# Kernel tuning notes

Measured on AMD Instinct MI355X. Metric: run time of the kernel, lower is better.

## Reference

```python
import jax, jax.numpy as jnp
import numpy as np

IN_DIM = 784   # 28*28
OUT_DIM = 16
NUM = 5        # grid intervals
K = 3          # spline order
HEADS = 10


def _make_grid():
    # pykan extended grid: linspace(-1,1,NUM+1) extended by K knots on each side
    h = 2.0 / NUM
    pts = np.arange(-K, NUM + K + 1, dtype=np.float32) * h - 1.0  # [NUM+2K+1]=12
    return jnp.asarray(np.broadcast_to(pts, (IN_DIM, pts.shape[0])))


def setup_inputs() -> dict:
    key = jax.random.key(0)
    ks = jax.random.split(key, 6)
    B = 16384
    x = jax.random.normal(ks[0], (B, 1, 28, 28), jnp.float32)
    grid = _make_grid()                                             # [784,12] (buffer)
    coef = jax.random.normal(ks[1], (HEADS, IN_DIM, OUT_DIM, NUM + K), jnp.float32) * 0.1
    scale_base = jax.random.normal(ks[2], (HEADS, IN_DIM, OUT_DIM), jnp.float32) * 0.1
    scale_sp = jnp.ones((HEADS, IN_DIM, OUT_DIM), jnp.float32)
    mask = jnp.ones((HEADS, IN_DIM, OUT_DIM), jnp.float32)
    w1 = jax.random.normal(ks[3], (HEADS, 8, OUT_DIM), jnp.float32) / np.sqrt(OUT_DIM)
    b1 = jnp.zeros((HEADS, 8), jnp.float32)
    w2 = jax.random.normal(ks[4], (HEADS, 1, 8), jnp.float32) / np.sqrt(8.0)
    b2 = jnp.zeros((HEADS, 1), jnp.float32)
    return dict(x=x, grid=grid, coef=coef, scale_base=scale_base, scale_sp=scale_sp,
                mask=mask, w1=w1, b1=b1, w2=w2, b2=b2)


def _b_spline(x, grid, k):
    # x: [B, D], grid: [D, G] -> bases [B, D, G-k-1] (Cox-de Boor recursion, pykan B_batch)
    xg = x[:, :, None]
    g = grid[None]
    B = ((xg >= g[:, :, :-1]) & (xg < g[:, :, 1:])).astype(x.dtype)
    for p in range(1, k + 1):
        left = (xg - g[:, :, :-(p + 1)]) / (g[:, :, p:-1] - g[:, :, :-(p + 1)])
        right = (g[:, :, p + 1:] - xg) / (g[:, :, p + 1:] - g[:, :, 1:-p])
        B = left * B[:, :, :-1] + right * B[:, :, 1:]
    return jnp.nan_to_num(B)


def reference(x, grid, coef, scale_base, scale_sp, mask, w1, b1, w2, b2):
    xf = x.reshape(x.shape[0], -1)                  # [B, 784]
    Bsp = _b_spline(xf, grid, K)                    # [B, 784, NUM+K]
    # KANLayer: y = sum_d mask*(scale_base*silu(x) + scale_sp*spline). Sum over d is
    # linear, so fold (scale_sp*mask) into coef to avoid the [B,H,784,16] intermediate.
    eff_coef = coef * (scale_sp * mask)[..., None]  # [H, 784, 16, NUM+K]
    y_sp = jnp.einsum('bdg,hdog->bho', Bsp, eff_coef)
    y_base = jnp.einsum('bd,hdo->bho', jax.nn.silu(xf), scale_base * mask)
    y = jnp.tanh(y_base + y_sp)                     # [B, H, 16] (nn.Tanh)
    h1 = jnp.tanh(jnp.einsum('bho,hpo->bhp', y, w1) + b1[None])   # Linear(16,8)+Tanh
    out = jnp.einsum('bhp,hqp->bhq', h1, w2) + b2[None]           # Linear(8,1)
    return out[..., 0]                              # concat of 10 heads -> [B, 10]
```

## Files before the change

### kernel.cpp

```cpp
#include <hip/hip_runtime.h>

#define IN_DIM 784
#define NF 9
#define NDB 25
#define NKC 225
#define KPAD (NKC*32)
#define BATCH 16384
#define NOUTC 160
#define NTILES 10
#define HEADS 10
#define KSPLIT 4
#define ROWB 576
#define CHUNKB 36864

typedef __attribute__((ext_vector_type(8))) short bf16x8;
typedef __attribute__((ext_vector_type(4))) float f32x4;
typedef __attribute__((ext_vector_type(4))) unsigned int u32x4;

__device__ __forceinline__ unsigned short f2bf(float f) {
    unsigned u = __builtin_bit_cast(unsigned, f);
    unsigned r = 0x7FFFu + ((u >> 16) & 1u);
    return (unsigned short)((u + r) >> 16);
}

__global__ void k_wprep(const float* __restrict__ coef, const float* __restrict__ scale_base,
                        const float* __restrict__ scale_sp, const float* __restrict__ mask,
                        unsigned short* __restrict__ Wp) {
    int tid = blockIdx.x * blockDim.x + threadIdx.x;
    if (tid >= KPAD * NOUTC) return;
    int frag = tid >> 9;
    int rem  = tid & 511;
    int l = rem >> 3, j = rem & 7;
    int kc = frag / NTILES, nt = frag - kc * NTILES;
    int db = kc / 9, c = kc - db * 9;
    int kk = ((l >> 4) << 3) + j;
    int d = db * 32 + kk;
    int n = nt * 16 + (l & 15);
    float v = 0.f;
    if (d < IN_DIM) {
        int h = n >> 4, o = n & 15;
        size_t base = ((size_t)h * IN_DIM + d) * 16 + o;
        float m = mask[base];
        v = (c == 0) ? scale_base[base] * m
                     : coef[base * 8 + (c - 1)] * scale_sp[base] * m;
    }
    Wp[tid] = f2bf(v);
}

template<int W>
__device__ __forceinline__ void do_units(const bf16x8* __restrict__ Bd,
                                         const char* __restrict__ lds,
                                         int q, int rr, f32x4* acc) {
    #pragma unroll
    for (int c = 0; c < 9; ++c) {
        bf16x8 aF[4];
        #pragma unroll
        for (int rg = 0; rg < 4; ++rg)
            aF[rg] = *(const bf16x8*)(lds + (rg * 16 + rr) * ROWB + c * 64 + q * 16);
        bf16x8 bcur;
        #pragma unroll
        for (int i = 0; i < 10; ++i) {
            const int tau = W * 10 + i;
            const int nt = tau >> 2, rg = tau & 3;
            if (i == 0 || rg == 0) bcur = Bd[c * (NTILES * 64) + nt * 64];
            acc[i] = __builtin_amdgcn_mfma_f32_16x16x32_bf16(aF[rg], bcur, acc[i], 0, 0, 0);
        }
    }
}

template<int W>
__device__ __forceinline__ void cwrite(float* __restrict__ pp, int row0g,
                                       int q, int rr, const f32x4* acc) {
    #pragma unroll
    for (int i = 0; i < 10; ++i) {
        const int tau = W * 10 + i;
        const int nt = tau >> 2, rg = tau & 3;
        #pragma unroll
        for (int ii = 0; ii < 4; ++ii)
            pp[(size_t)(row0g + rg * 16 + q * 4 + ii) * NOUTC + nt * 16 + rr] = acc[i][ii];
    }
}

__global__ void __launch_bounds__(256, 4) k_fused(const float* __restrict__ x,
                                                  const float* __restrict__ gridp,
                                                  const unsigned short* __restrict__ Wp,
                                                  float* __restrict__ part) {
    __shared__ char ldsb[CHUNKB];
    const int tid = threadIdx.x;
    const int l = tid & 63, wid = tid >> 6;
    const int q = l >> 4, rr = l & 15;
    const int row0g = blockIdx.x * 64;
    const int y = blockIdx.y;
    const int db0 = (y * NDB) >> 2, db1 = ((y + 1) * NDB) >> 2;

    const float g0 = gridp[0];
    const float ih = 1.f / (gridp[1] - g0);

    f32x4 acc[10];
    #pragma unroll
    for (int i = 0; i < 10; ++i) acc[i] = (f32x4){0.f, 0.f, 0.f, 0.f};

    const bf16x8* Bl = (const bf16x8*)Wp + l;
    const int sd = tid & 31;
    const int srow0 = tid >> 5;

    for (int db = db0; db < db1; ++db) {
        const u32x4 z = (u32x4){0u, 0u, 0u, 0u};
        #pragma unroll
        for (int i2 = 0; i2 < 9; ++i2) ((u32x4*)ldsb)[i2 * 256 + tid] = z;
        __syncthreads();

        const int d = db * 32 + sd;
        const bool valid = d < IN_DIM;
        #pragma unroll 4
        for (int it = 0; it < 8; ++it) {
            const int row = it * 8 + srow0;
            float xv = 0.f;
            if (valid) xv = x[(size_t)(row0g + row) * IN_DIM + d];
            const float u = (xv - g0) * ih;
            const float fm = floorf(u);
            const int m = (int)fm;
            const float t = u - fm;
            const float k6 = 0.16666667f;
            const float w0 = t * t * t * k6;
            const float w1 = fmaf(fmaf(fmaf(-3.f, t, 3.f), t, 3.f), t, 1.f) * k6;
            const float w2 = fmaf(fmaf(3.f, t, -6.f) * t, t, 4.f) * k6;
            const float omt = 1.f - t;
            const float w3 = omt * omt * omt * k6;
            const float den = 1.f + __expf(-xv);
            float inv; asm("v_rcp_f32 %0, %1" : "=v"(inv) : "v"(den));
            const float sil = xv * inv;
            if (valid) {
                char* rp = ldsb + row * ROWB;
                *(unsigned short*)(rp + sd * 2) = f2bf(sil);
                #pragma unroll
                for (int s = 0; s < 4; ++s) {
                    const int j = m - s;
                    const float w = (s == 0) ? w0 : (s == 1) ? w1 : (s == 2) ? w2 : w3;
                    if ((unsigned)j <= 7u)
                        *(unsigned short*)(rp + (j + 1) * 64 + sd * 2) = f2bf(w);
                }
            }
        }
        __syncthreads();

        const bf16x8* Bd = Bl + (size_t)db * (9 * NTILES * 64);
        switch (wid) {
            case 0:  do_units<0>(Bd, ldsb, q, rr, acc); break;
            case 1:  do_units<1>(Bd, ldsb, q, rr, acc); break;
            case 2:  do_units<2>(Bd, ldsb, q, rr, acc); break;
            default: do_units<3>(Bd, ldsb, q, rr, acc); break;
        }
        __syncthreads();
    }

    float* pp = part + (size_t)y * BATCH * NOUTC;
    switch (wid) {
        case 0:  cwrite<0>(pp, row0g, q, rr, acc); break;
        case 1:  cwrite<1>(pp, row0g, q, rr, acc); break;
        case 2:  cwrite<2>(pp, row0g, q, rr, acc); break;
        default: cwrite<3>(pp, row0g, q, rr, acc); break;
    }
}

__global__ void k_epi(const float* __restrict__ part, const float* __restrict__ w1,
                      const float* __restrict__ b1, const float* __restrict__ w2,
                      const float* __restrict__ b2, float* __restrict__ out) {
    int t = blockIdx.x * blockDim.x + threadIdx.x;
    if (t >= BATCH * HEADS) return;
    int b = t / HEADS;
    int h = t - b * HEADS;
    const f32x4* P = (const f32x4*)part;
    const int vbase = b * (NOUTC / 4) + h * 4;
    float y[16];
    #pragma unroll
    for (int c4 = 0; c4 < 4; ++c4) {
        f32x4 v = P[vbase + c4];
        #pragma unroll
        for (int s = 1; s < KSPLIT; ++s) {
            f32x4 v2 = P[(size_t)s * BATCH * (NOUTC / 4) + vbase + c4];
            v.x += v2.x; v.y += v2.y; v.z += v2.z; v.w += v2.w;
        }
        y[c4 * 4 + 0] = tanhf(v.x); y[c4 * 4 + 1] = tanhf(v.y);
        y[c4 * 4 + 2] = tanhf(v.z); y[c4 * 4 + 3] = tanhf(v.w);
    }
    float oacc = b2[h];
    #pragma unroll
    for (int p = 0; p < 8; ++p) {
        float a = b1[h * 8 + p];
        const float* wr = w1 + ((size_t)h * 8 + p) * 16;
        #pragma unroll
        for (int o = 0; o < 16; ++o) a = fmaf(y[o], wr[o], a);
        oacc = fmaf(tanhf(a), w2[h * 8 + p], oacc);
    }
    out[t] = oacc;
}

extern "C" void kernel_launch(void* const* d_in, const int* in_sizes, int n_in,
                              void* d_out, int out_size, void* d_ws, size_t ws_size,
                              hipStream_t stream) {
    const float* x          = (const float*)d_in[0];
    const float* gridp      = (const float*)d_in[1];
    const float* coef       = (const float*)d_in[2];
    const float* scale_base = (const float*)d_in[3];
    const float* scale_sp   = (const float*)d_in[4];
    const float* mask       = (const float*)d_in[5];
    const float* w1         = (const float*)d_in[6];
    const float* b1         = (const float*)d_in[7];
    const float* w2         = (const float*)d_in[8];
    const float* b2         = (const float*)d_in[9];
    float* out = (float*)d_out;

    char* ws = (char*)d_ws;
    float* part        = (float*)ws;
    unsigned short* Wp = (unsigned short*)(ws + 41943040);

    k_wprep<<<dim3((KPAD * NOUTC + 255) / 256), dim3(256), 0, stream>>>(coef, scale_base, scale_sp, mask, Wp);
    k_fused<<<dim3(BATCH / 64, KSPLIT), dim3(256), 0, stream>>>(x, gridp, Wp, part);
    k_epi  <<<dim3((BATCH * HEADS + 255) / 256), dim3(256), 0, stream>>>(part, w1, b1, w2, b2, out);
}
```

Measured before the change: 106.5 us.

## Switch to 32x32x16 MFMA with intra-block K-split across two waves

Replaces the 16x16x32 MFMA tiling over four waves with 32x32x16 MFMAs on two waves, each wave handling half of every 32-wide K chunk and all 160 outputs for 64 rows. The partial sums of the two waves are reduced through LDS before the global store. The weight prep is reordered to the new fragment layout and has the 1/6 spline constant folded in, which removes the per-element scaling. LDS rows are padded to reduce bank conflicts. Block size drops to 128 threads with larger accumulators per thread, which trades occupancy for fewer B-fragment loads and fewer MFMA issues.

```diff
diff --git a/kernel.cpp b/kernel.cpp
--- a/kernel.cpp
+++ b/kernel.cpp
@@ -1,20 +1,18 @@
 #include <hip/hip_runtime.h>
 
 #define IN_DIM 784
-#define NF 9
 #define NDB 25
-#define NKC 225
-#define KPAD (NKC*32)
+#define NUNITS (NDB*9)
 #define BATCH 16384
 #define NOUTC 160
-#define NTILES 10
 #define HEADS 10
 #define KSPLIT 4
-#define ROWB 576
-#define CHUNKB 36864
+#define ROWB 584
+#define CHUNKB (64*ROWB)
 
 typedef __attribute__((ext_vector_type(8))) short bf16x8;
 typedef __attribute__((ext_vector_type(4))) float f32x4;
+typedef __attribute__((ext_vector_type(16))) float f32x16;
 typedef __attribute__((ext_vector_type(4))) unsigned int u32x4;
 
 __device__ __forceinline__ unsigned short f2bf(float f) {
@@ -27,68 +25,36 @@
                         const float* __restrict__ scale_sp, const float* __restrict__ mask,
                         unsigned short* __restrict__ Wp) {
     int tid = blockIdx.x * blockDim.x + threadIdx.x;
-    if (tid >= KPAD * NOUTC) return;
+    if (tid >= NUNITS * 32 * NOUTC) return;
     int frag = tid >> 9;
     int rem  = tid & 511;
     int l = rem >> 3, j = rem & 7;
-    int kc = frag / NTILES, nt = frag - kc * NTILES;
+    int nt = frag % 5;
+    int t2 = frag / 5;
+    int kh = t2 & 1;
+    int kc = t2 >> 1;
     int db = kc / 9, c = kc - db * 9;
-    int kk = ((l >> 4) << 3) + j;
-    int d = db * 32 + kk;
-    int n = nt * 16 + (l & 15);
+    int d = db * 32 + kh * 16 + ((l >> 5) << 3) + j;
+    int n = nt * 32 + (l & 31);
     float v = 0.f;
     if (d < IN_DIM) {
         int h = n >> 4, o = n & 15;
         size_t base = ((size_t)h * IN_DIM + d) * 16 + o;
         float m = mask[base];
         v = (c == 0) ? scale_base[base] * m
-                     : coef[base * 8 + (c - 1)] * scale_sp[base] * m;
+                     : coef[base * 8 + (c - 1)] * scale_sp[base] * m * 0.16666667f;
     }
     Wp[tid] = f2bf(v);
 }
 
-template<int W>
-__device__ __forceinline__ void do_units(const bf16x8* __restrict__ Bd,
-                                         const char* __restrict__ lds,
-                                         int q, int rr, f32x4* acc) {
-    #pragma unroll
-    for (int c = 0; c < 9; ++c) {
-        bf16x8 aF[4];
-        #pragma unroll
-        for (int rg = 0; rg < 4; ++rg)
-            aF[rg] = *(const bf16x8*)(lds + (rg * 16 + rr) * ROWB + c * 64 + q * 16);
-        bf16x8 bcur;
-        #pragma unroll
-        for (int i = 0; i < 10; ++i) {
-            const int tau = W * 10 + i;
-            const int nt = tau >> 2, rg = tau & 3;
-            if (i == 0 || rg == 0) bcur = Bd[c * (NTILES * 64) + nt * 64];
-            acc[i] = __builtin_amdgcn_mfma_f32_16x16x32_bf16(aF[rg], bcur, acc[i], 0, 0, 0);
-        }
-    }
-}
-
-template<int W>
-__device__ __forceinline__ void cwrite(float* __restrict__ pp, int row0g,
-                                       int q, int rr, const f32x4* acc) {
-    #pragma unroll
-    for (int i = 0; i < 10; ++i) {
-        const int tau = W * 10 + i;
-        const int nt = tau >> 2, rg = tau & 3;
-        #pragma unroll
-        for (int ii = 0; ii < 4; ++ii)
-            pp[(size_t)(row0g + rg * 16 + q * 4 + ii) * NOUTC + nt * 16 + rr] = acc[i][ii];
-    }
-}
-
-__global__ void __launch_bounds__(256, 4) k_fused(const float* __restrict__ x,
+__global__ void __launch_bounds__(128, 2) k_fused(const float* __restrict__ x,
                                                   const float* __restrict__ gridp,
                                                   const unsigned short* __restrict__ Wp,
                                                   float* __restrict__ part) {
     __shared__ char ldsb[CHUNKB];
     const int tid = threadIdx.x;
-    const int l = tid & 63, wid = tid >> 6;
-    const int q = l >> 4, rr = l & 15;
+    const int l = tid & 63, kh = tid >> 6;
+    const int la = l & 31, lb = l >> 5;
     const int row0g = blockIdx.x * 64;
     const int y = blockIdx.y;
     const int db0 = (y * NDB) >> 2, db1 = ((y + 1) * NDB) >> 2;
@@ -96,37 +62,43 @@
     const float g0 = gridp[0];
     const float ih = 1.f / (gridp[1] - g0);
 
-    f32x4 acc[10];
+    f32x16 acc0[5], acc1[5];
     #pragma unroll
-    for (int i = 0; i < 10; ++i) acc[i] = (f32x4){0.f, 0.f, 0.f, 0.f};
-
-    const bf16x8* Bl = (const bf16x8*)Wp + l;
+    for (int i = 0; i < 5; ++i) {
+        #pragma unroll
+        for (int jj = 0; jj < 16; ++jj) { acc0[i][jj] = 0.f; acc1[i][jj] = 0.f; }
+    }
+
     const int sd = tid & 31;
     const int srow0 = tid >> 5;
+    const char* aAddr = ldsb + la * ROWB + kh * 32 + lb * 16;
+    const bf16x8* Bl = (const bf16x8*)Wp + l;
 
     for (int db = db0; db < db1; ++db) {
-        const u32x4 z = (u32x4){0u, 0u, 0u, 0u};
-        #pragma unroll
-        for (int i2 = 0; i2 < 9; ++i2) ((u32x4*)ldsb)[i2 * 256 + tid] = z;
+        const u32x4 z4 = (u32x4){0u, 0u, 0u, 0u};
+        #pragma unroll
+        for (int i = 0; i < 19; ++i) {
+            int off = (i * 128 + tid) * 16;
+            if (off < CHUNKB) *(u32x4*)(ldsb + off) = z4;
+        }
         __syncthreads();
 
         const int d = db * 32 + sd;
         const bool valid = d < IN_DIM;
+        const float* xp = x + (size_t)row0g * IN_DIM + d;
         #pragma unroll 4
-        for (int it = 0; it < 8; ++it) {
-            const int row = it * 8 + srow0;
-            float xv = 0.f;
-            if (valid) xv = x[(size_t)(row0g + row) * IN_DIM + d];
+        for (int it = 0; it < 16; ++it) {
+            const int row = it * 4 + srow0;
+            float xv = valid ? xp[(size_t)row * IN_DIM] : 0.f;
             const float u = (xv - g0) * ih;
             const float fm = floorf(u);
             const int m = (int)fm;
             const float t = u - fm;
-            const float k6 = 0.16666667f;
-            const float w0 = t * t * t * k6;
-            const float w1 = fmaf(fmaf(fmaf(-3.f, t, 3.f), t, 3.f), t, 1.f) * k6;
-            const float w2 = fmaf(fmaf(3.f, t, -6.f) * t, t, 4.f) * k6;
+            const float w0 = t * t * t;
+            const float w1 = fmaf(fmaf(fmaf(-3.f, t, 3.f), t, 3.f), t, 1.f);
+            const float w2 = fmaf(fmaf(3.f, t, -6.f) * t, t, 4.f);
             const float omt = 1.f - t;
-            const float w3 = omt * omt * omt * k6;
+            const float w3 = omt * omt * omt;
             const float den = 1.f + __expf(-xv);
             float inv; asm("v_rcp_f32 %0, %1" : "=v"(inv) : "v"(den));
             const float sil = xv * inv;
@@ -144,23 +116,67 @@
         }
         __syncthreads();
 
-        const bf16x8* Bd = Bl + (size_t)db * (9 * NTILES * 64);
-        switch (wid) {
-            case 0:  do_units<0>(Bd, ldsb, q, rr, acc); break;
-            case 1:  do_units<1>(Bd, ldsb, q, rr, acc); break;
-            case 2:  do_units<2>(Bd, ldsb, q, rr, acc); break;
-            default: do_units<3>(Bd, ldsb, q, rr, acc); break;
+        const size_t ub = (size_t)(db * 9) * 10 * 64;
+        #pragma unroll
+        for (int c = 0; c < 9; ++c) {
+            const size_t bi = ub + (size_t)((c * 2 + kh) * 5) * 64;
+            const bf16x8 b0 = Bl[bi];
+            const bf16x8 b1 = Bl[bi + 64];
+            const bf16x8 b2 = Bl[bi + 128];
+            const bf16x8 b3 = Bl[bi + 192];
+            const bf16x8 b4 = Bl[bi + 256];
+            const bf16x8 a0 = *(const bf16x8*)(aAddr + c * 64);
+            const bf16x8 a1 = *(const bf16x8*)(aAddr + 32 * ROWB + c * 64);
+            acc0[0] = __builtin_amdgcn_mfma_f32_32x32x16_bf16(a0, b0, acc0[0], 0, 0, 0);
+            acc1[0] = __builtin_amdgcn_mfma_f32_32x32x16_bf16(a1, b0, acc1[0], 0, 0, 0);
+            acc0[1] = __builtin_amdgcn_mfma_f32_32x32x16_bf16(a0, b1, acc0[1], 0, 0, 0);
+            acc1[1] = __builtin_amdgcn_mfma_f32_32x32x16_bf16(a1, b1, acc1[1], 0, 0, 0);
+            acc0[2] = __builtin_amdgcn_mfma_f32_32x32x16_bf16(a0, b2, acc0[2], 0, 0, 0);
+            acc1[2] = __builtin_amdgcn_mfma_f32_32x32x16_bf16(a1, b2, acc1[2], 0, 0, 0);
+            acc0[3] = __builtin_amdgcn_mfma_f32_32x32x16_bf16(a0, b3, acc0[3], 0, 0, 0);
+            acc1[3] = __builtin_amdgcn_mfma_f32_32x32x16_bf16(a1, b3, acc1[3], 0, 0, 0);
+            acc0[4] = __builtin_amdgcn_mfma_f32_32x32x16_bf16(a0, b4, acc0[4], 0, 0, 0);
+            acc1[4] = __builtin_amdgcn_mfma_f32_32x32x16_bf16(a1, b4, acc1[4], 0, 0, 0);
         }
         __syncthreads();
     }
 
     float* pp = part + (size_t)y * BATCH * NOUTC;
-    switch (wid) {
-        case 0:  cwrite<0>(pp, row0g, q, rr, acc); break;
-        case 1:  cwrite<1>(pp, row0g, q, rr, acc); break;
-        case 2:  cwrite<2>(pp, row0g, q, rr, acc); break;
-        default: cwrite<3>(pp, row0g, q, rr, acc); break;
-    }
+#define REDUCE_STORE(ACC, RG)                                                   \
+    {                                                                           \
+        if (kh == 1) {                                                          \
+            _Pragma("unroll")                                                   \
+            for (int nt = 0; nt < 5; ++nt) {                                    \
+                _Pragma("unroll")                                               \
+                for (int g = 0; g < 4; ++g) {                                   \
+                    f32x4 v = (f32x4){ACC[nt][g*4+0], ACC[nt][g*4+1],           \
+                                      ACC[nt][g*4+2], ACC[nt][g*4+3]};          \
+                    *(f32x4*)(ldsb + nt * 5120 + l * 80 + g * 16) = v;          \
+                }                                                               \
+            }                                                                   \
+        }                                                                       \
+        __syncthreads();                                                        \
+        if (kh == 0) {                                                          \
+            _Pragma("unroll")                                                   \
+            for (int nt = 0; nt < 5; ++nt) {                                    \
+                _Pragma("unroll")                                               \
+                for (int g = 0; g < 4; ++g) {                                   \
+                    f32x4 v = *(const f32x4*)(ldsb + nt * 5120 + l * 80 + g * 16); \
+                    _Pragma("unroll")                                           \
+                    for (int ii = 0; ii < 4; ++ii) {                            \
+                        const int r = g * 4 + ii;                               \
+                        const int rl = (r & 3) + 8 * (r >> 2) + 4 * lb;         \
+                        pp[(size_t)(row0g + RG * 32 + rl) * NOUTC + nt * 32 + la] \
+                            = ACC[nt][r] + v[ii];                               \
+                    }                                                           \
+                }                                                               \
+            }                                                                   \
+        }                                                                       \
+        __syncthreads();                                                        \
+    }
+    REDUCE_STORE(acc0, 0)
+    REDUCE_STORE(acc1, 1)
+#undef REDUCE_STORE
 }
 
 __global__ void k_epi(const float* __restrict__ part, const float* __restrict__ w1,
@@ -215,7 +231,7 @@
     float* part        = (float*)ws;
     unsigned short* Wp = (unsigned short*)(ws + 41943040);
 
-    k_wprep<<<dim3((KPAD * NOUTC + 255) / 256), dim3(256), 0, stream>>>(coef, scale_base, scale_sp, mask, Wp);
-    k_fused<<<dim3(BATCH / 64, KSPLIT), dim3(256), 0, stream>>>(x, gridp, Wp, part);
+    k_wprep<<<dim3((NUNITS * 32 * NOUTC + 255) / 256), dim3(256), 0, stream>>>(coef, scale_base, scale_sp, mask, Wp);
+    k_fused<<<dim3(BATCH / 64, KSPLIT), dim3(128), 0, stream>>>(x, gridp, Wp, part);
     k_epi  <<<dim3((BATCH * HEADS + 255) / 256), dim3(256), 0, stream>>>(part, w1, b1, w2, b2, out);
 }
```

After: 146.2 us. 1.37x slower.

## Restructure fused KAN GEMM to 8 waves with prefetched x and dense LDS scatter

Applied to the files above, without the earlier changes.

Doubles the block to 512 threads and splits the 64x160 output tile so each wave owns one 16-row group and half the columns (5 accumulators instead of 10). The next x chunk is loaded into registers before the MFMA phase so global loads overlap compute, and the per-chunk LDS zeroing pass and its barrier are removed by writing all 8 basis slots explicitly, with zeros where no basis applies. The 1/6 spline factor moves into the prepared weights, and LDS rows are padded to 584 bytes to reduce bank conflicts. In exchange each wave reuses one A fragment per B load instead of four, so B traffic from global/L2 per wave goes up, and the larger block may lower occupancy.

```diff
diff --git a/kernel.cpp b/kernel.cpp
--- a/kernel.cpp
+++ b/kernel.cpp
@@ -1,21 +1,18 @@
 #include <hip/hip_runtime.h>
 
 #define IN_DIM 784
-#define NF 9
 #define NDB 25
-#define NKC 225
-#define KPAD (NKC*32)
+#define NUNITS (NDB*9)
 #define BATCH 16384
 #define NOUTC 160
-#define NTILES 10
+#define NT16 10
 #define HEADS 10
 #define KSPLIT 4
-#define ROWB 576
-#define CHUNKB 36864
+#define ROWB 584
+#define CHUNKB (64*ROWB)
 
 typedef __attribute__((ext_vector_type(8))) short bf16x8;
 typedef __attribute__((ext_vector_type(4))) float f32x4;
-typedef __attribute__((ext_vector_type(4))) unsigned int u32x4;
 
 __device__ __forceinline__ unsigned short f2bf(float f) {
     unsigned u = __builtin_bit_cast(unsigned, f);
@@ -27,11 +24,11 @@
                         const float* __restrict__ scale_sp, const float* __restrict__ mask,
                         unsigned short* __restrict__ Wp) {
     int tid = blockIdx.x * blockDim.x + threadIdx.x;
-    if (tid >= KPAD * NOUTC) return;
+    if (tid >= NUNITS * 32 * NOUTC) return;
     int frag = tid >> 9;
     int rem  = tid & 511;
     int l = rem >> 3, j = rem & 7;
-    int kc = frag / NTILES, nt = frag - kc * NTILES;
+    int kc = frag / 10, nt = frag - kc * 10;
     int db = kc / 9, c = kc - db * 9;
     int kk = ((l >> 4) << 3) + j;
     int d = db * 32 + kk;
@@ -42,124 +39,110 @@
         size_t base = ((size_t)h * IN_DIM + d) * 16 + o;
         float m = mask[base];
         v = (c == 0) ? scale_base[base] * m
-                     : coef[base * 8 + (c - 1)] * scale_sp[base] * m;
+                     : coef[base * 8 + (c - 1)] * scale_sp[base] * m * 0.16666667f;
     }
     Wp[tid] = f2bf(v);
 }
 
-template<int W>
-__device__ __forceinline__ void do_units(const bf16x8* __restrict__ Bd,
-                                         const char* __restrict__ lds,
-                                         int q, int rr, f32x4* acc) {
-    #pragma unroll
-    for (int c = 0; c < 9; ++c) {
-        bf16x8 aF[4];
-        #pragma unroll
-        for (int rg = 0; rg < 4; ++rg)
-            aF[rg] = *(const bf16x8*)(lds + (rg * 16 + rr) * ROWB + c * 64 + q * 16);
-        bf16x8 bcur;
-        #pragma unroll
-        for (int i = 0; i < 10; ++i) {
-            const int tau = W * 10 + i;
-            const int nt = tau >> 2, rg = tau & 3;
-            if (i == 0 || rg == 0) bcur = Bd[c * (NTILES * 64) + nt * 64];
-            acc[i] = __builtin_amdgcn_mfma_f32_16x16x32_bf16(aF[rg], bcur, acc[i], 0, 0, 0);
-        }
-    }
-}
-
-template<int W>
-__device__ __forceinline__ void cwrite(float* __restrict__ pp, int row0g,
-                                       int q, int rr, const f32x4* acc) {
-    #pragma unroll
-    for (int i = 0; i < 10; ++i) {
-        const int tau = W * 10 + i;
-        const int nt = tau >> 2, rg = tau & 3;
-        #pragma unroll
-        for (int ii = 0; ii < 4; ++ii)
-            pp[(size_t)(row0g + rg * 16 + q * 4 + ii) * NOUTC + nt * 16 + rr] = acc[i][ii];
-    }
-}
-
-__global__ void __launch_bounds__(256, 4) k_fused(const float* __restrict__ x,
+__global__ void __launch_bounds__(512, 4) k_fused(const float* __restrict__ x,
                                                   const float* __restrict__ gridp,
                                                   const unsigned short* __restrict__ Wp,
                                                   float* __restrict__ part) {
     __shared__ char ldsb[CHUNKB];
     const int tid = threadIdx.x;
     const int l = tid & 63, wid = tid >> 6;
-    const int q = l >> 4, rr = l & 15;
+    const int rr = l & 15, q = l >> 4;
+    const int rg = wid >> 1, nh = wid & 1;
+    const int sd = tid & 31, srg = tid >> 5;
     const int row0g = blockIdx.x * 64;
     const int y = blockIdx.y;
     const int db0 = (y * NDB) >> 2, db1 = ((y + 1) * NDB) >> 2;
 
     const float g0 = gridp[0];
     const float ih = 1.f / (gridp[1] - g0);
-
-    f32x4 acc[10];
-    #pragma unroll
-    for (int i = 0; i < 10; ++i) acc[i] = (f32x4){0.f, 0.f, 0.f, 0.f};
-
-    const bf16x8* Bl = (const bf16x8*)Wp + l;
-    const int sd = tid & 31;
-    const int srow0 = tid >> 5;
-
-    for (int db = db0; db < db1; ++db) {
-        const u32x4 z = (u32x4){0u, 0u, 0u, 0u};
-        #pragma unroll
-        for (int i2 = 0; i2 < 9; ++i2) ((u32x4*)ldsb)[i2 * 256 + tid] = z;
-        __syncthreads();
-
+    const float nihg0 = -g0 * ih;
+
+    f32x4 acc[5];
+    #pragma unroll
+    for (int i = 0; i < 5; ++i) acc[i] = (f32x4){0.f, 0.f, 0.f, 0.f};
+
+    const char* wpb = (const char*)Wp;
+    float xv[4];
+
+    auto loadX = [&](int db) {
         const int d = db * 32 + sd;
-        const bool valid = d < IN_DIM;
-        #pragma unroll 4
-        for (int it = 0; it < 8; ++it) {
-            const int row = it * 8 + srow0;
-            float xv = 0.f;
-            if (valid) xv = x[(size_t)(row0g + row) * IN_DIM + d];
-            const float u = (xv - g0) * ih;
+        const int dc = d < IN_DIM ? d : IN_DIM - 1;
+        const float* xp = x + (size_t)(row0g + srg) * IN_DIM + dc;
+        #pragma unroll
+        for (int it = 0; it < 4; ++it) xv[it] = xp[(size_t)it * 16 * IN_DIM];
+    };
+
+    auto evalScatter = [&]() {
+        #pragma unroll
+        for (int it = 0; it < 4; ++it) {
+            const float v = xv[it];
+            const float u = fmaf(v, ih, nihg0);
             const float fm = floorf(u);
             const int m = (int)fm;
             const float t = u - fm;
-            const float k6 = 0.16666667f;
-            const float w0 = t * t * t * k6;
-            const float w1 = fmaf(fmaf(fmaf(-3.f, t, 3.f), t, 3.f), t, 1.f) * k6;
-            const float w2 = fmaf(fmaf(3.f, t, -6.f) * t, t, 4.f) * k6;
+            const float t2 = t * t;
+            const float w0 = t2 * t;
+            const float w1 = fmaf(fmaf(fmaf(-3.f, t, 3.f), t, 3.f), t, 1.f);
+            const float w2 = fmaf(fmaf(3.f, t, -6.f) * t, t, 4.f);
             const float omt = 1.f - t;
-            const float w3 = omt * omt * omt * k6;
-            const float den = 1.f + __expf(-xv);
+            const float w3 = omt * omt * omt;
+            const float den = 1.f + __expf(-v);
             float inv; asm("v_rcp_f32 %0, %1" : "=v"(inv) : "v"(den));
-            const float sil = xv * inv;
-            if (valid) {
-                char* rp = ldsb + row * ROWB;
-                *(unsigned short*)(rp + sd * 2) = f2bf(sil);
-                #pragma unroll
-                for (int s = 0; s < 4; ++s) {
-                    const int j = m - s;
-                    const float w = (s == 0) ? w0 : (s == 1) ? w1 : (s == 2) ? w2 : w3;
-                    if ((unsigned)j <= 7u)
-                        *(unsigned short*)(rp + (j + 1) * 64 + sd * 2) = f2bf(w);
+            const float sil = v * inv;
+            char* rb = ldsb + (it * 16 + srg) * ROWB + sd * 2;
+            *(unsigned short*)rb = f2bf(sil);
+            #pragma unroll
+            for (int s = 0; s < 8; ++s) {
+                const int ms = m - s;
+                const unsigned off = (((unsigned)ms & 7u) << 6) + 64u;
+                float wv = 0.f;
+                if (s <= 3) {
+                    const float wsel = (s == 0) ? w0 : (s == 1) ? w1 : (s == 2) ? w2 : w3;
+                    wv = ((unsigned)ms <= 7u) ? wsel : 0.f;
                 }
+                *(unsigned short*)(rb + off) = f2bf(wv);
             }
         }
+    };
+
+    loadX(db0);
+    for (int db = db0; db < db1; ++db) {
         __syncthreads();
-
-        const bf16x8* Bd = Bl + (size_t)db * (9 * NTILES * 64);
-        switch (wid) {
-            case 0:  do_units<0>(Bd, ldsb, q, rr, acc); break;
-            case 1:  do_units<1>(Bd, ldsb, q, rr, acc); break;
-            case 2:  do_units<2>(Bd, ldsb, q, rr, acc); break;
-            default: do_units<3>(Bd, ldsb, q, rr, acc); break;
+        evalScatter();
+        if (db + 1 < db1) loadX(db + 1);
+        __syncthreads();
+
+        const char* arow = ldsb + (rg * 16 + rr) * ROWB + q * 16;
+        const char* bb = wpb + (size_t)db * 92160 + nh * 5120 + l * 16;
+        #pragma unroll
+        for (int c = 0; c < 9; ++c) {
+            const bf16x8 a = *(const bf16x8*)(arow + c * 64);
+            const char* bc = bb + c * 10240;
+            const bf16x8 b0 = *(const bf16x8*)(bc);
+            const bf16x8 b1 = *(const bf16x8*)(bc + 1024);
+            const bf16x8 b2 = *(const bf16x8*)(bc + 2048);
+            const bf16x8 b3 = *(const bf16x8*)(bc + 3072);
+            const bf16x8 b4 = *(const bf16x8*)(bc + 4096);
+            acc[0] = __builtin_amdgcn_mfma_f32_16x16x32_bf16(a, b0, acc[0], 0, 0, 0);
+            acc[1] = __builtin_amdgcn_mfma_f32_16x16x32_bf16(a, b1, acc[1], 0, 0, 0);
+            acc[2] = __builtin_amdgcn_mfma_f32_16x16x32_bf16(a, b2, acc[2], 0, 0, 0);
+            acc[3] = __builtin_amdgcn_mfma_f32_16x16x32_bf16(a, b3, acc[3], 0, 0, 0);
+            acc[4] = __builtin_amdgcn_mfma_f32_16x16x32_bf16(a, b4, acc[4], 0, 0, 0);
         }
-        __syncthreads();
     }
 
     float* pp = part + (size_t)y * BATCH * NOUTC;
-    switch (wid) {
-        case 0:  cwrite<0>(pp, row0g, q, rr, acc); break;
-        case 1:  cwrite<1>(pp, row0g, q, rr, acc); break;
-        case 2:  cwrite<2>(pp, row0g, q, rr, acc); break;
-        default: cwrite<3>(pp, row0g, q, rr, acc); break;
+    #pragma unroll
+    for (int ntl = 0; ntl < 5; ++ntl) {
+        const int col = (nh * 5 + ntl) * 16 + rr;
+        #pragma unroll
+        for (int ii = 0; ii < 4; ++ii)
+            pp[(size_t)(row0g + rg * 16 + q * 4 + ii) * NOUTC + col] = acc[ntl][ii];
     }
 }
 
@@ -215,7 +198,7 @@
     float* part        = (float*)ws;
     unsigned short* Wp = (unsigned short*)(ws + 41943040);
 
-    k_wprep<<<dim3((KPAD * NOUTC + 255) / 256), dim3(256), 0, stream>>>(coef, scale_base, scale_sp, mask, Wp);
-    k_fused<<<dim3(BATCH / 64, KSPLIT), dim3(256), 0, stream>>>(x, gridp, Wp, part);
+    k_wprep<<<dim3((NUNITS * 32 * NOUTC + 255) / 256), dim3(256), 0, stream>>>(coef, scale_base, scale_sp, mask, Wp);
+    k_fused<<<dim3(BATCH / 64, KSPLIT), dim3(512), 0, stream>>>(x, gridp, Wp, part);
     k_epi  <<<dim3((BATCH * HEADS + 255) / 256), dim3(256), 0, stream>>>(part, w1, b1, w2, b2, out);
 }
```

Result: slower. 129.3 us (+21.5%).
